# Kernel tuning notes

Measured on AMD Instinct MI355X. Metric: run time of the kernel, lower is better.

Reference implementation:

```python
import jax, jax.numpy as jnp
import numpy as np

# ---- static config (matches init_kwargs) ----
B = 32          # batch
CTX = 128       # context_dim
N_FRAMES = 128
N_SAMPLES = 32768
N_EVENTS = 16
CH = 256        # channels
WIN = 512       # window_size
HOP = WIN // 2  # 256
N_COEFFS = WIN // 2 + 1   # 257
TOTAL_COEFFS = N_COEFFS * 2  # 514


def _hann(n):
    # periodic Hann window (torch.hann_window default)
    i = jnp.arange(n, dtype=jnp.float32)
    return 0.5 * (1.0 - jnp.cos(2.0 * jnp.pi * i / n))


def _forward(param, times, noise, pos, proj_w, proj_b,
             w0, b0, w1, b1, w2, b2, w_out, b_out):
    # proj: [B, CTX] -> [B, CH]
    x = param @ proj_w.T + proj_b
    x = x[:, None, :] + pos                      # [B, N_FRAMES, CH] (pos broadcast)
    # LinearOutputStack: 3 hidden layers w/ leaky_relu(0.2), then output layer
    for w, b in ((w0, b0), (w1, b1), (w2, b2)):
        x = jax.nn.leaky_relu(x @ w.T + b, 0.2)
    x = x @ w_out.T + b_out                      # [B, N_FRAMES, 514]
    x = x.reshape(B, N_FRAMES, N_COEFFS, 2)
    mags = jnp.abs(x[..., 0])                    # [B, F, 257]
    phase = x[..., 1]
    # phase jitter: base phase of ones perturbed by uniform(-1,1) noise
    phase = 1.0 + phase * noise
    # mag/phase recomposition: per-frequency phase increment accumulated over frames
    freqs = jnp.linspace(0.0, 1.0, N_COEFFS)
    p = jnp.cumsum(phase * freqs * jnp.pi, axis=1)
    spec = mags * jnp.exp(1j * p)                # complex [B, F, 257]
    frames = jnp.fft.irfft(spec, n=WIN, axis=-1)  # [B, F, 512]
    frames = frames * _hann(WIN)
    total = (N_FRAMES - 1) * HOP + WIN
    idx = (jnp.arange(N_FRAMES) * HOP)[:, None] + jnp.arange(WIN)  # [F, 512]
    sig = jnp.zeros((B, total), frames.dtype).at[:, idx].add(frames)
    sig = sig[:, :N_SAMPLES]                     # [B, N_SAMPLES]
    # DiracScheduler (pre_sparse): upsample-with-holes frame-resolution diracs
    step = N_SAMPLES // N_FRAMES                 # 256
    up = jnp.zeros((B, N_EVENTS, N_SAMPLES), sig.dtype).at[:, :, ::step].set(times)
    # fft convolve event signal with dirac trains (zero-padded, linear conv)
    n2 = 2 * N_SAMPLES
    S = jnp.fft.rfft(sig, n=n2)[:, None, :]      # [B, 1, n2//2+1]
    T = jnp.fft.rfft(up, n=n2)                   # [B, E, n2//2+1]
    out = jnp.fft.irfft(S * T, n=n2)[..., :N_SAMPLES]
    return out                                   # [B, N_EVENTS, N_SAMPLES]


def setup_inputs() -> dict:
    key = jax.random.key(0)
    ks = jax.random.split(key, 16)
    s = 0.02
    param = jax.random.normal(ks[0], (B, CTX), jnp.float32)
    # sparse dirac times: one event position per (batch, event) at frame resolution
    posn = jax.random.randint(ks[1], (B, N_EVENTS), 0, N_FRAMES)
    amps = jax.random.uniform(ks[2], (B, N_EVENTS), jnp.float32, 0.1, 1.0)
    times = jax.nn.one_hot(posn, N_FRAMES, dtype=jnp.float32) * amps[..., None]
    noise = jax.random.uniform(ks[3], (B, N_FRAMES, N_COEFFS), jnp.float32, -1.0, 1.0)
    pos = jax.random.uniform(ks[4], (1, N_FRAMES, CH), jnp.float32, -0.01, 0.01)
    proj_w = jax.random.normal(ks[5], (CH, CTX), jnp.float32) * s
    proj_b = jnp.zeros((CH,), jnp.float32)
    w0 = jax.random.normal(ks[6], (CH, CH), jnp.float32) * s
    b0 = jnp.zeros((CH,), jnp.float32)
    w1 = jax.random.normal(ks[7], (CH, CH), jnp.float32) * s
    b1 = jnp.zeros((CH,), jnp.float32)
    w2 = jax.random.normal(ks[8], (CH, CH), jnp.float32) * s
    b2 = jnp.zeros((CH,), jnp.float32)
    w_out = jax.random.normal(ks[9], (TOTAL_COEFFS, CH), jnp.float32) * s
    b_out = jnp.zeros((TOTAL_COEFFS,), jnp.float32)
    return dict(param=param, times=times, noise=noise, pos=pos,
                proj_w=proj_w, proj_b=proj_b, w0=w0, b0=b0, w1=w1, b1=b1,
                w2=w2, b2=b2, w_out=w_out, b_out=b_out)


def reference(param, times, noise, pos, proj_w, proj_b,
              w0, b0, w1, b1, w2, b2, w_out, b_out):
    return _forward(param, times, noise, pos, proj_w, proj_b,
                    w0, b0, w1, b1, w2, b2, w_out, b_out)
```

## Files before the change

### kernel.cpp

```cpp
#include <hip/hip_runtime.h>
#include <cstddef>

typedef unsigned short u16;
typedef __bf16 bf16x8 __attribute__((ext_vector_type(8)));
typedef float f32x4 __attribute__((ext_vector_type(4)));

constexpr int B_   = 32;
constexpr int CTX_ = 128;
constexpr int NF_  = 128;
constexpr int NS_  = 32768;
constexpr int NE_  = 16;
constexpr int CH_  = 256;
constexpr int NC_  = 257;
constexpr int TC_  = 514;
constexpr int ROWS_ = B_ * NF_;
constexpr int CHUNK_ = 8;
constexpr int NCH_ = NF_ / CHUNK_;
constexpr int KE_ = 288;
constexpr int K3MLP_ = 768;
constexpr int K3IR_ = 896;
constexpr float PI_ = 3.14159265358979323846f;

__device__ __forceinline__ float lrelu(float v) { return v > 0.f ? v : 0.2f * v; }
__device__ __forceinline__ u16 f2bf(float x) {
    unsigned u = __float_as_uint(x);
    return (u16)((u + 0x7FFFu + ((u >> 16) & 1u)) >> 16);
}
__device__ __forceinline__ float bf2f(u16 h) { return __uint_as_float(((unsigned)h) << 16); }

__global__ __launch_bounds__(256) void prep_kernel(
    const float* __restrict__ param, const float* __restrict__ pw,
    const float* __restrict__ pb, const float* __restrict__ pos,
    const float* __restrict__ w0, const float* __restrict__ w1,
    const float* __restrict__ w2, const float* __restrict__ wo,
    const float* __restrict__ times,
    u16* __restrict__ Tt3, u16* __restrict__ W1_3, u16* __restrict__ W2_3,
    u16* __restrict__ WO_3, int* __restrict__ cnt, float2* __restrict__ taps,
    float* __restrict__ U, float* __restrict__ V)
{
    int blk = blockIdx.x;
    int tid = threadIdx.x;
    if (blk < 1792) {
        int idx = blk * 256 + tid;
        int z = idx / (256 * K3IR_);
        int r = idx - z * (256 * K3IR_);
        int n = r / K3IR_, col = r - n * K3IR_;
        u16 outv = 0;
        if (col < 864) {
            int seg = col / KE_;
            int j = col - seg * KE_;
            float val = 0.f;
            if (z == 0) {
                if (j < 129) {
                    int k = 2 * j;
                    float w = (k == 0 || k == 256) ? 1.f : 2.f;
                    int m = (k * n) & 511;
                    val = w * (1.f / 512.f) * cosf((float)m * (PI_ / 256.f));
                } else if (j < 258) {
                    int kk = 2 * (j - 129);
                    float w = (kk == 0 || kk == 256) ? 1.f : 2.f;
                    int m = (kk * n) & 511;
                    val = -w * (1.f / 512.f) * sinf((float)m * (PI_ / 256.f));
                }
            } else {
                if (j < 128) {
                    int k = 2 * j + 1;
                    int m = (k * n) & 511;
                    val = 2.f * (1.f / 512.f) * cosf((float)m * (PI_ / 256.f));
                } else if (j < 256) {
                    int kk = 2 * (j - 128) + 1;
                    int m = (kk * n) & 511;
                    val = -2.f * (1.f / 512.f) * sinf((float)m * (PI_ / 256.f));
                }
            }
            u16 h = f2bf(val);
            outv = (seg < 2) ? h : f2bf(val - bf2f(h));
        }
        Tt3[idx] = outv;
    } else if (blk < 2880) {
        int row = blk - 1792;
        int k = tid;
        float v;
        u16* p;
        if (row < 256) {
            v = w1[row * 256 + k];
            p = W1_3 + (size_t)row * K3MLP_;
        } else if (row < 512) {
            v = w2[(row - 256) * 256 + k];
            p = W2_3 + (size_t)(row - 256) * K3MLP_;
        } else {
            int n = row - 512;
            v = (n < TC_) ? wo[n * 256 + k] : 0.f;
            p = WO_3 + (size_t)n * K3MLP_;
        }
        u16 h = f2bf(v), lo = f2bf(v - bf2f(h));
        p[k] = h; p[256 + k] = h; p[512 + k] = lo;
    } else if (blk < 3392) {
        int be = blk - 2880;
        __shared__ int c;
        if (tid == 0) c = 0;
        __syncthreads();
        if (tid < NF_) {
            float v = times[(size_t)be * NF_ + tid];
            if (v != 0.f) {
                int slot = atomicAdd(&c, 1);
                taps[(size_t)be * NF_ + slot] = make_float2((float)tid, v);
            }
        }
        __syncthreads();
        if (tid == 0) cnt[be] = c;
    } else if (blk < 3424) {
        int b = blk - 3392;
        __shared__ float ly[256];
        {
            const float* pr = param + b * CTX_;
            const float* wr = pw + tid * CTX_;
            float s = 0.f;
            #pragma unroll 4
            for (int j = 0; j < CTX_; ++j) s += pr[j] * wr[j];
            ly[tid] = s + pb[tid];
        }
        __syncthreads();
        {
            const float* wn = w0 + tid * CH_;
            float s = 0.f;
            #pragma unroll 4
            for (int c2 = 0; c2 < CH_; ++c2) s += ly[c2] * wn[c2];
            U[b * CH_ + tid] = s;
        }
    } else {
        int f = blk - 3424;
        const float* pf = pos + f * CH_;
        const float* wn = w0 + tid * CH_;
        float s = 0.f;
        #pragma unroll 4
        for (int c2 = 0; c2 < CH_; ++c2) s += pf[c2] * wn[c2];
        V[f * CH_ + tid] = s;
    }
}

__global__ void fuse1_kernel(const float* __restrict__ U, const float* __restrict__ V,
                             const float* __restrict__ b0, u16* __restrict__ H3) {
    int idx = blockIdx.x * 256 + threadIdx.x;
    int c = idx & 255;
    int row = idx >> 8;
    int b = row >> 7, f = row & 127;
    float v = lrelu(U[b * CH_ + c] + V[f * CH_ + c] + b0[c]);
    u16 h = f2bf(v), lo = f2bf(v - bf2f(h));
    u16* p = H3 + (size_t)row * K3MLP_;
    p[c] = h; p[256 + c] = lo; p[512 + c] = h;
}

template<int EPI, int K3>
__global__ __launch_bounds__(128) void mfgemm(
    const u16* __restrict__ A3, const u16* __restrict__ B3,
    const float* __restrict__ bias, void* __restrict__ Cout,
    int N, int lda, int ldb, int ldc,
    size_t sAz, size_t sBz, size_t sCz)
{
    A3 += (size_t)blockIdx.z * sAz;
    B3 += (size_t)blockIdx.z * sBz;
    const int tid = threadIdx.x;
    const int m0 = blockIdx.y * 32, n0 = blockIdx.x * 64;
    __shared__ __align__(16) u16 Als[2 * 32 * 64];
    __shared__ __align__(16) u16 Bls[2 * 64 * 64];
    const int sr = tid >> 2;
    const int sc = (tid & 3) * 16;
    const u16* ga  = A3 + (size_t)(m0 + sr) * lda + sc;
    const u16* gb0 = B3 + (size_t)(n0 + sr) * ldb + sc;
    const u16* gb1 = B3 + (size_t)(n0 + 32 + sr) * ldb + sc;
    const int xr = (sr & 7) << 4;
    const int loA0 = sr * 128 + ((sc * 2) ^ xr);
    const int loA1 = sr * 128 + ((sc * 2 + 16) ^ xr);
    const int loB0 = sr * 128 + ((sc * 2) ^ xr);
    const int loB1 = sr * 128 + ((sc * 2 + 16) ^ xr);
    const int loB2 = (sr + 32) * 128 + ((sc * 2) ^ xr);
    const int loB3 = (sr + 32) * 128 + ((sc * 2 + 16) ^ xr);
    const int wv = tid >> 6, lane = tid & 63;
    const int wc = wv * 32;
    const int lr = lane & 15;
    const int lkb = (lane >> 4) * 16;
    const int xf = (lr & 7) << 4;
    const int raf0 = lr * 128, raf1 = (16 + lr) * 128;
    const int rbf0 = (wc + lr) * 128, rbf1 = (wc + 16 + lr) * 128;
    f32x4 acc00 = {0.f, 0.f, 0.f, 0.f}, acc01 = acc00, acc10 = acc00, acc11 = acc00;

    uint4 pa0, pa1, pb0, pb1, pb2, pb3;
    uint4 qa0, qa1, qb0, qb1, qb2, qb3;
    auto loadP = [&](int kt) {
        pa0 = *(const uint4*)(ga + kt);  pa1 = *(const uint4*)(ga + kt + 8);
        pb0 = *(const uint4*)(gb0 + kt); pb1 = *(const uint4*)(gb0 + kt + 8);
        pb2 = *(const uint4*)(gb1 + kt); pb3 = *(const uint4*)(gb1 + kt + 8);
    };
    auto loadQ = [&](int kt) {
        qa0 = *(const uint4*)(ga + kt);  qa1 = *(const uint4*)(ga + kt + 8);
        qb0 = *(const uint4*)(gb0 + kt); qb1 = *(const uint4*)(gb0 + kt + 8);
        qb2 = *(const uint4*)(gb1 + kt); qb3 = *(const uint4*)(gb1 + kt + 8);
    };
    auto compute = [&](int p) {
        const char* pa = (const char*)Als + p * 4096;
        const char* pb = (const char*)Bls + p * 8192;
        #pragma unroll
        for (int s = 0; s < 2; ++s) {
            int kb = (s * 64 + lkb) ^ xf;
            bf16x8 a0 = *(const bf16x8*)(pa + raf0 + kb);
            bf16x8 a1 = *(const bf16x8*)(pa + raf1 + kb);
            bf16x8 b0 = *(const bf16x8*)(pb + rbf0 + kb);
            bf16x8 b1 = *(const bf16x8*)(pb + rbf1 + kb);
            acc00 = __builtin_amdgcn_mfma_f32_16x16x32_bf16(a0, b0, acc00, 0, 0, 0);
            acc01 = __builtin_amdgcn_mfma_f32_16x16x32_bf16(a0, b1, acc01, 0, 0, 0);
            acc10 = __builtin_amdgcn_mfma_f32_16x16x32_bf16(a1, b0, acc10, 0, 0, 0);
            acc11 = __builtin_amdgcn_mfma_f32_16x16x32_bf16(a1, b1, acc11, 0, 0, 0);
        }
    };
    auto stage = [&](int p, const uint4& a0, const uint4& a1, const uint4& b0,
                     const uint4& b1, const uint4& b2, const uint4& b3) {
        char* ab = (char*)Als + p * 4096;
        char* bb = (char*)Bls + p * 8192;
        *(uint4*)(ab + loA0) = a0; *(uint4*)(ab + loA1) = a1;
        *(uint4*)(bb + loB0) = b0; *(uint4*)(bb + loB1) = b1;
        *(uint4*)(bb + loB2) = b2; *(uint4*)(bb + loB3) = b3;
    };
    loadP(0);
    loadQ(64);
    int p = 0;
    #pragma unroll
    for (int kt = 0; kt < K3; kt += 128) {
        stage(p, pa0, pa1, pb0, pb1, pb2, pb3);
        __syncthreads();
        if (kt + 128 < K3) loadP(kt + 128);
        compute(p);
        p ^= 1;
        stage(p, qa0, qa1, qb0, qb1, qb2, qb3);
        __syncthreads();
        if (kt + 192 < K3) loadQ(kt + 192);
        compute(p);
        p ^= 1;
    }
    const int er = (lane >> 4) * 4;
    const int ec = lane & 15;
    auto emit = [&](const f32x4& A, int mi, int ni) {
        #pragma unroll
        for (int r = 0; r < 4; ++r) {
            int m = m0 + mi * 16 + er + r;
            int n = n0 + wc + ni * 16 + ec;
            float v = A[r];
            if (EPI == 0) {
                v = lrelu(v + bias[n]);
                u16 h = f2bf(v), lo = f2bf(v - bf2f(h));
                u16* p2 = (u16*)Cout + (size_t)m * ldc + n;
                p2[0] = h; p2[256] = lo; p2[512] = h;
            } else if (EPI == 1) {
                if (n < N) ((float*)Cout)[(size_t)m * ldc + n] = v + bias[n];
            } else {
                float* cf = (float*)Cout + (size_t)blockIdx.z * sCz;
                cf[(size_t)m * ldc + n] = v;
            }
        }
    };
    emit(acc00, 0, 0); emit(acc01, 0, 1); emit(acc10, 1, 0); emit(acc11, 1, 1);
}

__global__ void scan1_kernel(const float* __restrict__ raw, const float* __restrict__ noise,
                             double* __restrict__ sums) {
    int b = blockIdx.x, c = blockIdx.y;
    int k = threadIdx.x;
    if (k >= NC_) return;
    float kf = (float)k * (PI_ / 256.f);
    double s = 0.0;
    #pragma unroll
    for (int j = 0; j < CHUNK_; ++j) {
        int row = b * NF_ + c * CHUNK_ + j;
        float2 v = *(const float2*)(raw + (size_t)row * TC_ + 2 * k);
        float d = (1.f + v.y * noise[(size_t)row * NC_ + k]) * kf;
        s += (double)d;
    }
    sums[((size_t)(b * NCH_ + c)) * NC_ + k] = s;
}

__global__ void scan2_kernel(const float* __restrict__ raw, const float* __restrict__ noise,
                             const double* __restrict__ sums,
                             u16* __restrict__ AB3e, u16* __restrict__ AB3o) {
    int b = blockIdx.x, c = blockIdx.y;
    int k = threadIdx.x;
    if (k >= NC_) {
        int t = k - NC_;
        for (int idx = t; idx < 250; idx += 63) {
            int col;
            u16* base;
            if (idx < 122) {
                col = (idx < 90) ? ((idx / 30) * KE_ + 258 + (idx % 30)) : (864 + (idx - 90));
                base = AB3e;
            } else {
                int u = idx - 122;
                col = (u < 96) ? ((u / 32) * KE_ + 256 + (u % 32)) : (864 + (u - 96));
                base = AB3o;
            }
            for (int j = 0; j < CHUNK_; ++j)
                base[(size_t)(b * NF_ + c * CHUNK_ + j) * K3IR_ + col] = 0;
        }
        return;
    }
    double p = 0.0;
    for (int cc = 0; cc < c; ++cc)
        p += sums[((size_t)(b * NCH_ + cc)) * NC_ + k];
    float kf = (float)k * (PI_ / 256.f);
    int half = k >> 1;
    bool even = (k & 1) == 0;
    int ccol = half;
    int scol = even ? (129 + half) : (128 + half);
    u16* dst = even ? AB3e : AB3o;
    for (int j = 0; j < CHUNK_; ++j) {
        int row = b * NF_ + c * CHUNK_ + j;
        float2 v = *(const float2*)(raw + (size_t)row * TC_ + 2 * k);
        float d = (1.f + v.y * noise[(size_t)row * NC_ + k]) * kf;
        p += (double)d;
        float m = fabsf(v.x);
        float sn, cs;
        sincosf((float)p, &sn, &cs);
        float a = m * cs, bb = m * sn;
        u16* pr = dst + (size_t)row * K3IR_;
        u16 ha = f2bf(a), la = f2bf(a - bf2f(ha));
        pr[ccol] = ha; pr[KE_ + ccol] = la; pr[2 * KE_ + ccol] = ha;
        u16 hb = f2bf(bb), lb = f2bf(bb - bf2f(hb));
        pr[scol] = hb; pr[KE_ + scol] = lb; pr[2 * KE_ + scol] = hb;
    }
}

__global__ __launch_bounds__(256) void conv2_kernel(const float* __restrict__ E,
                                                    const float* __restrict__ O,
                                                    const int* __restrict__ cnt,
                                                    const float2* __restrict__ taps,
                                                    float* __restrict__ out) {
    int be = blockIdx.y;
    int b = be >> 4;
    int n = cnt[be];
    int t = blockIdx.x * 2048 + (int)threadIdx.x * 8;
    int r0 = t & 255;
    float hr[8], hr2[8];
    #pragma unroll
    for (int j = 0; j < 8; ++j) {
        float cj = cosf((float)(r0 + j) * (PI_ / 256.f));
        hr[j]  = 0.5f - 0.5f * cj;
        hr2[j] = 0.5f + 0.5f * cj;
    }
    float acc[8] = {};
    for (int i = 0; i < n; ++i) {
        float2 ka = taps[(size_t)be * NF_ + i];
        int s0 = t - ((int)ka.x << 8);
        if (s0 < 0) continue;
        float amp = ka.y;
        int q = s0 >> 8;
        size_t row = (size_t)(b * NF_ + q) * 256 + r0;
        float4 e0 = *(const float4*)(E + row);
        float4 e1 = *(const float4*)(E + row + 4);
        float4 o0 = *(const float4*)(O + row);
        float4 o1 = *(const float4*)(O + row + 4);
        float sv[8];
        sv[0] = hr[0] * (e0.x + o0.x); sv[1] = hr[1] * (e0.y + o0.y);
        sv[2] = hr[2] * (e0.z + o0.z); sv[3] = hr[3] * (e0.w + o0.w);
        sv[4] = hr[4] * (e1.x + o1.x); sv[5] = hr[5] * (e1.y + o1.y);
        sv[6] = hr[6] * (e1.z + o1.z); sv[7] = hr[7] * (e1.w + o1.w);
        if (q > 0) {
            float4 pe0 = *(const float4*)(E + row - 256);
            float4 pe1 = *(const float4*)(E + row - 252);
            float4 po0 = *(const float4*)(O + row - 256);
            float4 po1 = *(const float4*)(O + row - 252);
            sv[0] += hr2[0] * (pe0.x - po0.x); sv[1] += hr2[1] * (pe0.y - po0.y);
            sv[2] += hr2[2] * (pe0.z - po0.z); sv[3] += hr2[3] * (pe0.w - po0.w);
            sv[4] += hr2[4] * (pe1.x - po1.x); sv[5] += hr2[5] * (pe1.y - po1.y);
            sv[6] += hr2[6] * (pe1.z - po1.z); sv[7] += hr2[7] * (pe1.w - po1.w);
        }
        #pragma unroll
        for (int j = 0; j < 8; ++j) acc[j] += amp * sv[j];
    }
    float* op = out + (size_t)be * NS_ + t;
    *(float4*)op = make_float4(acc[0], acc[1], acc[2], acc[3]);
    *(float4*)(op + 4) = make_float4(acc[4], acc[5], acc[6], acc[7]);
}

extern "C" void kernel_launch(void* const* d_in, const int* in_sizes, int n_in,
                              void* d_out, int out_size, void* d_ws, size_t ws_size,
                              hipStream_t stream) {
    const float* param  = (const float*)d_in[0];
    const float* times  = (const float*)d_in[1];
    const float* noise  = (const float*)d_in[2];
    const float* pos    = (const float*)d_in[3];
    const float* proj_w = (const float*)d_in[4];
    const float* proj_b = (const float*)d_in[5];
    const float* w0 = (const float*)d_in[6];
    const float* b0 = (const float*)d_in[7];
    const float* w1 = (const float*)d_in[8];
    const float* b1 = (const float*)d_in[9];
    const float* w2 = (const float*)d_in[10];
    const float* b2 = (const float*)d_in[11];
    const float* w_out = (const float*)d_in[12];
    const float* b_out = (const float*)d_in[13];
    float* out = (float*)d_out;
    float* ws = (float*)d_ws;

    constexpr size_t U_F    = 32 * 256;
    constexpr size_t V_F    = 128 * 256;
    constexpr size_t H3_F   = (size_t)ROWS_ * K3MLP_ / 2;
    constexpr size_t W3_F   = (size_t)256 * K3MLP_ / 2;
    constexpr size_t WO3_F  = (size_t)576 * K3MLP_ / 2;
    constexpr size_t RAW_F  = (size_t)ROWS_ * TC_;
    constexpr size_t AB3_F  = 2 * (size_t)ROWS_ * K3IR_ / 2;
    constexpr size_t TT3_F  = 2 * (size_t)256 * K3IR_ / 2;
    constexpr size_t EO_F   = 2 * (size_t)ROWS_ * 256;
    constexpr size_t SUMS_F = (size_t)B_ * NCH_ * NC_ * 2;

    size_t cur = 0;
    float* U    = ws + cur;                 cur += U_F;
    float* V    = ws + cur;                 cur += V_F;
    u16*  H1_3  = (u16*)(ws + cur);         cur += H3_F;
    u16*  H2_3  = (u16*)(ws + cur);         cur += H3_F;
    u16*  H3_3  = (u16*)(ws + cur);         cur += H3_F;
    u16*  W1_3  = (u16*)(ws + cur);         cur += W3_F;
    u16*  W2_3  = (u16*)(ws + cur);         cur += W3_F;
    u16*  WO_3  = (u16*)(ws + cur);         cur += WO3_F;
    float* RAW  = ws + cur;                 cur += RAW_F;
    u16*  AB3   = (u16*)(ws + cur);         cur += AB3_F;
    u16*  AB3e  = AB3;
    u16*  AB3o  = AB3 + (size_t)ROWS_ * K3IR_;
    u16*  Tt3   = (u16*)(ws + cur);         cur += TT3_F;
    float* EO   = ws + cur;                 cur += EO_F;
    double* SUMS = (double*)(ws + cur);     cur += SUMS_F;
    int*   CNT  = (int*)(ws + cur);         cur += 512;
    float2* TAPS = (float2*)(ws + cur);

    prep_kernel<<<3552, 256, 0, stream>>>(param, proj_w, proj_b, pos, w0, w1, w2, w_out,
                                          times, Tt3, W1_3, W2_3, WO_3, CNT, TAPS, U, V);
    fuse1_kernel<<<ROWS_ * CH_ / 256, 256, 0, stream>>>(U, V, b0, H1_3);
    mfgemm<0, K3MLP_><<<dim3(4, 128, 1), 128, 0, stream>>>(H1_3, W1_3, b1, H2_3, 256,
                                                           K3MLP_, K3MLP_, K3MLP_, 0, 0, 0);
    mfgemm<0, K3MLP_><<<dim3(4, 128, 1), 128, 0, stream>>>(H2_3, W2_3, b2, H3_3, 256,
                                                           K3MLP_, K3MLP_, K3MLP_, 0, 0, 0);
    mfgemm<1, K3MLP_><<<dim3(9, 128, 1), 128, 0, stream>>>(H3_3, WO_3, b_out, RAW, TC_,
                                                           K3MLP_, K3MLP_, TC_, 0, 0, 0);
    dim3 gS(B_, NCH_);
    scan1_kernel<<<gS, 320, 0, stream>>>(RAW, noise, SUMS);
    scan2_kernel<<<gS, 320, 0, stream>>>(RAW, noise, SUMS, AB3e, AB3o);
    mfgemm<2, K3IR_><<<dim3(4, 128, 2), 128, 0, stream>>>(AB3, Tt3, nullptr, EO, 256,
                                                          K3IR_, K3IR_, 256,
                                                          (size_t)ROWS_ * K3IR_,
                                                          (size_t)256 * K3IR_,
                                                          (size_t)ROWS_ * 256);
    dim3 gC(NS_ / 2048, B_ * NE_);
    conv2_kernel<<<gC, 256, 0, stream>>>(EO, EO + (size_t)ROWS_ * 256, CNT, TAPS, out);
}
```

Before: 106.4 us.

## Store split-bf16 operands as hi/lo pairs and synthesize the third K segment

The three-term split-bf16 GEMM operands (hi·hi + lo·hi + hi·lo) used to be stored physically tripled along K. They are now stored as just [hi, lo] per row, and the GEMM remaps the K index so the third segment re-reads the first A or B segment. This cuts workspace writes in the prep, scan and epilogue kernels and the global footprint the GEMMs read, while keeping the same MMA work. The IRFFT segment also grows from 288 to 320 columns, which adds padded K work. The twiddle table now uses a shared-memory cosine LUT instead of per-element sin/cos.

```diff
diff --git a/kernel.cpp b/kernel.cpp
--- a/kernel.cpp
+++ b/kernel.cpp
@@ -16,9 +16,12 @@
 constexpr int ROWS_ = B_ * NF_;
 constexpr int CHUNK_ = 8;
 constexpr int NCH_ = NF_ / CHUNK_;
-constexpr int KE_ = 288;
 constexpr int K3MLP_ = 768;
-constexpr int K3IR_ = 896;
+constexpr int SEGM_ = 256;
+constexpr int K3IR_ = 960;
+constexpr int SEGI_ = 320;
+constexpr int PIRW_ = 2 * SEGI_;
+constexpr int PMLW_ = 2 * SEGM_;
 constexpr float PI_ = 3.14159265358979323846f;
 
 __device__ __forceinline__ float lrelu(float v) { return v > 0.f ? v : 0.2f * v; }
@@ -34,69 +37,69 @@
     const float* __restrict__ w0, const float* __restrict__ w1,
     const float* __restrict__ w2, const float* __restrict__ wo,
     const float* __restrict__ times,
-    u16* __restrict__ Tt3, u16* __restrict__ W1_3, u16* __restrict__ W2_3,
-    u16* __restrict__ WO_3, int* __restrict__ cnt, float2* __restrict__ taps,
+    u16* __restrict__ Tt, u16* __restrict__ W1p, u16* __restrict__ W2p,
+    u16* __restrict__ WOp, int* __restrict__ cnt, float2* __restrict__ taps,
     float* __restrict__ U, float* __restrict__ V)
 {
     int blk = blockIdx.x;
     int tid = threadIdx.x;
-    if (blk < 1792) {
+    if (blk < 1280) {
+        __shared__ float lut[512];
+        lut[tid]       = cosf((float)tid * (PI_ / 256.f));
+        lut[tid + 256] = cosf((float)(tid + 256) * (PI_ / 256.f));
+        __syncthreads();
         int idx = blk * 256 + tid;
-        int z = idx / (256 * K3IR_);
-        int r = idx - z * (256 * K3IR_);
-        int n = r / K3IR_, col = r - n * K3IR_;
-        u16 outv = 0;
-        if (col < 864) {
-            int seg = col / KE_;
-            int j = col - seg * KE_;
-            float val = 0.f;
-            if (z == 0) {
-                if (j < 129) {
-                    int k = 2 * j;
-                    float w = (k == 0 || k == 256) ? 1.f : 2.f;
-                    int m = (k * n) & 511;
-                    val = w * (1.f / 512.f) * cosf((float)m * (PI_ / 256.f));
-                } else if (j < 258) {
-                    int kk = 2 * (j - 129);
-                    float w = (kk == 0 || kk == 256) ? 1.f : 2.f;
-                    int m = (kk * n) & 511;
-                    val = -w * (1.f / 512.f) * sinf((float)m * (PI_ / 256.f));
-                }
-            } else {
-                if (j < 128) {
-                    int k = 2 * j + 1;
-                    int m = (k * n) & 511;
-                    val = 2.f * (1.f / 512.f) * cosf((float)m * (PI_ / 256.f));
-                } else if (j < 256) {
-                    int kk = 2 * (j - 128) + 1;
-                    int m = (kk * n) & 511;
-                    val = -2.f * (1.f / 512.f) * sinf((float)m * (PI_ / 256.f));
-                }
+        int z = idx / (256 * PIRW_);
+        int r = idx - z * (256 * PIRW_);
+        int n = r / PIRW_, c = r - n * PIRW_;
+        bool hiplane = c < SEGI_;
+        int j = hiplane ? c : c - SEGI_;
+        float val = 0.f;
+        if (z == 0) {
+            if (j < 129) {
+                int k = 2 * j;
+                float w = (k == 0 || k == 256) ? 1.f : 2.f;
+                int m = (k * n) & 511;
+                val = w * (1.f / 512.f) * lut[m];
+            } else if (j < 258) {
+                int kk = 2 * (j - 129);
+                float w = (kk == 0 || kk == 256) ? 1.f : 2.f;
+                int m = (kk * n) & 511;
+                val = -w * (1.f / 512.f) * lut[(m - 128) & 511];
             }
-            u16 h = f2bf(val);
-            outv = (seg < 2) ? h : f2bf(val - bf2f(h));
-        }
-        Tt3[idx] = outv;
-    } else if (blk < 2880) {
-        int row = blk - 1792;
+        } else {
+            if (j < 128) {
+                int k = 2 * j + 1;
+                int m = (k * n) & 511;
+                val = 2.f * (1.f / 512.f) * lut[m];
+            } else if (j < 256) {
+                int kk = 2 * (j - 128) + 1;
+                int m = (kk * n) & 511;
+                val = -2.f * (1.f / 512.f) * lut[(m - 128) & 511];
+            }
+        }
+        u16 h = f2bf(val);
+        Tt[idx] = hiplane ? h : f2bf(val - bf2f(h));
+    } else if (blk < 2368) {
+        int row = blk - 1280;
         int k = tid;
         float v;
         u16* p;
         if (row < 256) {
             v = w1[row * 256 + k];
-            p = W1_3 + (size_t)row * K3MLP_;
+            p = W1p + (size_t)row * PMLW_;
         } else if (row < 512) {
             v = w2[(row - 256) * 256 + k];
-            p = W2_3 + (size_t)(row - 256) * K3MLP_;
+            p = W2p + (size_t)(row - 256) * PMLW_;
         } else {
             int n = row - 512;
             v = (n < TC_) ? wo[n * 256 + k] : 0.f;
-            p = WO_3 + (size_t)n * K3MLP_;
-        }
-        u16 h = f2bf(v), lo = f2bf(v - bf2f(h));
-        p[k] = h; p[256 + k] = h; p[512 + k] = lo;
-    } else if (blk < 3392) {
-        int be = blk - 2880;
+            p = WOp + (size_t)n * PMLW_;
+        }
+        u16 h = f2bf(v);
+        p[k] = h; p[256 + k] = f2bf(v - bf2f(h));
+    } else if (blk < 2880) {
+        int be = blk - 2368;
         __shared__ int c;
         if (tid == 0) c = 0;
         __syncthreads();
@@ -109,8 +112,8 @@
         }
         __syncthreads();
         if (tid == 0) cnt[be] = c;
-    } else if (blk < 3424) {
-        int b = blk - 3392;
+    } else if (blk < 2912) {
+        int b = blk - 2880;
         __shared__ float ly[256];
         {
             const float* pr = param + b * CTX_;
@@ -129,7 +132,7 @@
             U[b * CH_ + tid] = s;
         }
     } else {
-        int f = blk - 3424;
+        int f = blk - 2912;
         const float* pf = pos + f * CH_;
         const float* wn = w0 + tid * CH_;
         float s = 0.f;
@@ -140,24 +143,25 @@
 }
 
 __global__ void fuse1_kernel(const float* __restrict__ U, const float* __restrict__ V,
-                             const float* __restrict__ b0, u16* __restrict__ H3) {
+                             const float* __restrict__ b0, u16* __restrict__ Hp) {
     int idx = blockIdx.x * 256 + threadIdx.x;
     int c = idx & 255;
     int row = idx >> 8;
     int b = row >> 7, f = row & 127;
     float v = lrelu(U[b * CH_ + c] + V[f * CH_ + c] + b0[c]);
-    u16 h = f2bf(v), lo = f2bf(v - bf2f(h));
-    u16* p = H3 + (size_t)row * K3MLP_;
-    p[c] = h; p[256 + c] = lo; p[512 + c] = h;
-}
-
-template<int EPI, int K3>
+    u16 h = f2bf(v);
+    u16* p = Hp + (size_t)row * PMLW_;
+    p[c] = h; p[256 + c] = f2bf(v - bf2f(h));
+}
+
+template<int EPI, int K3, int SEG>
 __global__ __launch_bounds__(128) void mfgemm(
     const u16* __restrict__ A3, const u16* __restrict__ B3,
     const float* __restrict__ bias, void* __restrict__ Cout,
     int N, int lda, int ldb, int ldc,
     size_t sAz, size_t sBz, size_t sCz)
 {
+    constexpr int NSTEP = K3 / 64;
     A3 += (size_t)blockIdx.z * sAz;
     B3 += (size_t)blockIdx.z * sBz;
     const int tid = threadIdx.x;
@@ -172,8 +176,6 @@
     const int xr = (sr & 7) << 4;
     const int loA0 = sr * 128 + ((sc * 2) ^ xr);
     const int loA1 = sr * 128 + ((sc * 2 + 16) ^ xr);
-    const int loB0 = sr * 128 + ((sc * 2) ^ xr);
-    const int loB1 = sr * 128 + ((sc * 2 + 16) ^ xr);
     const int loB2 = (sr + 32) * 128 + ((sc * 2) ^ xr);
     const int loB3 = (sr + 32) * 128 + ((sc * 2 + 16) ^ xr);
     const int wv = tid >> 6, lane = tid & 63;
@@ -187,15 +189,19 @@
 
     uint4 pa0, pa1, pb0, pb1, pb2, pb3;
     uint4 qa0, qa1, qb0, qb1, qb2, qb3;
+    auto kA = [](int kt) { return kt >= 2 * SEG ? kt - 2 * SEG : kt; };
+    auto kB = [](int kt) { return kt >= SEG ? kt - SEG : kt; };
     auto loadP = [&](int kt) {
-        pa0 = *(const uint4*)(ga + kt);  pa1 = *(const uint4*)(ga + kt + 8);
-        pb0 = *(const uint4*)(gb0 + kt); pb1 = *(const uint4*)(gb0 + kt + 8);
-        pb2 = *(const uint4*)(gb1 + kt); pb3 = *(const uint4*)(gb1 + kt + 8);
+        int a = kA(kt), b = kB(kt);
+        pa0 = *(const uint4*)(ga + a);  pa1 = *(const uint4*)(ga + a + 8);
+        pb0 = *(const uint4*)(gb0 + b); pb1 = *(const uint4*)(gb0 + b + 8);
+        pb2 = *(const uint4*)(gb1 + b); pb3 = *(const uint4*)(gb1 + b + 8);
     };
     auto loadQ = [&](int kt) {
-        qa0 = *(const uint4*)(ga + kt);  qa1 = *(const uint4*)(ga + kt + 8);
-        qb0 = *(const uint4*)(gb0 + kt); qb1 = *(const uint4*)(gb0 + kt + 8);
-        qb2 = *(const uint4*)(gb1 + kt); qb3 = *(const uint4*)(gb1 + kt + 8);
+        int a = kA(kt), b = kB(kt);
+        qa0 = *(const uint4*)(ga + a);  qa1 = *(const uint4*)(ga + a + 8);
+        qb0 = *(const uint4*)(gb0 + b); qb1 = *(const uint4*)(gb0 + b + 8);
+        qb2 = *(const uint4*)(gb1 + b); qb3 = *(const uint4*)(gb1 + b + 8);
     };
     auto compute = [&](int p) {
         const char* pa = (const char*)Als + p * 4096;
@@ -218,23 +224,25 @@
         char* ab = (char*)Als + p * 4096;
         char* bb = (char*)Bls + p * 8192;
         *(uint4*)(ab + loA0) = a0; *(uint4*)(ab + loA1) = a1;
-        *(uint4*)(bb + loB0) = b0; *(uint4*)(bb + loB1) = b1;
+        *(uint4*)(bb + loA0) = b0; *(uint4*)(bb + loA1) = b1;
         *(uint4*)(bb + loB2) = b2; *(uint4*)(bb + loB3) = b3;
     };
     loadP(0);
-    loadQ(64);
+    if (NSTEP > 1) loadQ(64);
     int p = 0;
     #pragma unroll
-    for (int kt = 0; kt < K3; kt += 128) {
-        stage(p, pa0, pa1, pb0, pb1, pb2, pb3);
-        __syncthreads();
-        if (kt + 128 < K3) loadP(kt + 128);
-        compute(p);
-        p ^= 1;
-        stage(p, qa0, qa1, qb0, qb1, qb2, qb3);
-        __syncthreads();
-        if (kt + 192 < K3) loadQ(kt + 192);
-        compute(p);
+    for (int i = 0; i < NSTEP; ++i) {
+        if ((i & 1) == 0) {
+            stage(p, pa0, pa1, pb0, pb1, pb2, pb3);
+            __syncthreads();
+            if (i + 2 < NSTEP) loadP((i + 2) * 64);
+            compute(p);
+        } else {
+            stage(p, qa0, qa1, qb0, qb1, qb2, qb3);
+            __syncthreads();
+            if (i + 2 < NSTEP) loadQ((i + 2) * 64);
+            compute(p);
+        }
         p ^= 1;
     }
     const int er = (lane >> 4) * 4;
@@ -247,9 +255,9 @@
             float v = A[r];
             if (EPI == 0) {
                 v = lrelu(v + bias[n]);
-                u16 h = f2bf(v), lo = f2bf(v - bf2f(h));
+                u16 h = f2bf(v);
                 u16* p2 = (u16*)Cout + (size_t)m * ldc + n;
-                p2[0] = h; p2[256] = lo; p2[512] = h;
+                p2[0] = h; p2[256] = f2bf(v - bf2f(h));
             } else if (EPI == 1) {
                 if (n < N) ((float*)Cout)[(size_t)m * ldc + n] = v + bias[n];
             } else {
@@ -280,24 +288,20 @@
 
 __global__ void scan2_kernel(const float* __restrict__ raw, const float* __restrict__ noise,
                              const double* __restrict__ sums,
-                             u16* __restrict__ AB3e, u16* __restrict__ AB3o) {
+                             u16* __restrict__ ABe, u16* __restrict__ ABo) {
     int b = blockIdx.x, c = blockIdx.y;
     int k = threadIdx.x;
     if (k >= NC_) {
         int t = k - NC_;
-        for (int idx = t; idx < 250; idx += 63) {
+        for (int idx = t; idx < 252; idx += 63) {
             int col;
             u16* base;
-            if (idx < 122) {
-                col = (idx < 90) ? ((idx / 30) * KE_ + 258 + (idx % 30)) : (864 + (idx - 90));
-                base = AB3e;
-            } else {
-                int u = idx - 122;
-                col = (u < 96) ? ((u / 32) * KE_ + 256 + (u % 32)) : (864 + (u - 96));
-                base = AB3o;
-            }
+            if (idx < 62)       { col = 258 + idx;              base = ABe; }
+            else if (idx < 124) { col = SEGI_ + 258 + (idx - 62);  base = ABe; }
+            else if (idx < 188) { col = 256 + (idx - 124);       base = ABo; }
+            else                { col = SEGI_ + 256 + (idx - 188); base = ABo; }
             for (int j = 0; j < CHUNK_; ++j)
-                base[(size_t)(b * NF_ + c * CHUNK_ + j) * K3IR_ + col] = 0;
+                base[(size_t)(b * NF_ + c * CHUNK_ + j) * PIRW_ + col] = 0;
         }
         return;
     }
@@ -309,7 +313,7 @@
     bool even = (k & 1) == 0;
     int ccol = half;
     int scol = even ? (129 + half) : (128 + half);
-    u16* dst = even ? AB3e : AB3o;
+    u16* dst = even ? ABe : ABo;
     for (int j = 0; j < CHUNK_; ++j) {
         int row = b * NF_ + c * CHUNK_ + j;
         float2 v = *(const float2*)(raw + (size_t)row * TC_ + 2 * k);
@@ -319,11 +323,11 @@
         float sn, cs;
         sincosf((float)p, &sn, &cs);
         float a = m * cs, bb = m * sn;
-        u16* pr = dst + (size_t)row * K3IR_;
-        u16 ha = f2bf(a), la = f2bf(a - bf2f(ha));
-        pr[ccol] = ha; pr[KE_ + ccol] = la; pr[2 * KE_ + ccol] = ha;
-        u16 hb = f2bf(bb), lb = f2bf(bb - bf2f(hb));
-        pr[scol] = hb; pr[KE_ + scol] = lb; pr[2 * KE_ + scol] = hb;
+        u16* pr = dst + (size_t)row * PIRW_;
+        u16 ha = f2bf(a);
+        pr[ccol] = ha; pr[SEGI_ + ccol] = f2bf(a - bf2f(ha));
+        u16 hb = f2bf(bb);
+        pr[scol] = hb; pr[SEGI_ + scol] = f2bf(bb - bf2f(hb));
     }
 }
 
@@ -401,51 +405,51 @@
 
     constexpr size_t U_F    = 32 * 256;
     constexpr size_t V_F    = 128 * 256;
-    constexpr size_t H3_F   = (size_t)ROWS_ * K3MLP_ / 2;
-    constexpr size_t W3_F   = (size_t)256 * K3MLP_ / 2;
-    constexpr size_t WO3_F  = (size_t)576 * K3MLP_ / 2;
+    constexpr size_t HP_F   = (size_t)ROWS_ * PMLW_ / 2;
+    constexpr size_t W_F    = (size_t)256 * PMLW_ / 2;
+    constexpr size_t WO_F   = (size_t)576 * PMLW_ / 2;
     constexpr size_t RAW_F  = (size_t)ROWS_ * TC_;
-    constexpr size_t AB3_F  = 2 * (size_t)ROWS_ * K3IR_ / 2;
-    constexpr size_t TT3_F  = 2 * (size_t)256 * K3IR_ / 2;
+    constexpr size_t ABP_F  = 2 * (size_t)ROWS_ * PIRW_ / 2;
+    constexpr size_t TTP_F  = 2 * (size_t)256 * PIRW_ / 2;
     constexpr size_t EO_F   = 2 * (size_t)ROWS_ * 256;
     constexpr size_t SUMS_F = (size_t)B_ * NCH_ * NC_ * 2;
 
     size_t cur = 0;
     float* U    = ws + cur;                 cur += U_F;
     float* V    = ws + cur;                 cur += V_F;
-    u16*  H1_3  = (u16*)(ws + cur);         cur += H3_F;
-    u16*  H2_3  = (u16*)(ws + cur);         cur += H3_F;
-    u16*  H3_3  = (u16*)(ws + cur);         cur += H3_F;
-    u16*  W1_3  = (u16*)(ws + cur);         cur += W3_F;
-    u16*  W2_3  = (u16*)(ws + cur);         cur += W3_F;
-    u16*  WO_3  = (u16*)(ws + cur);         cur += WO3_F;
+    u16*  H1p   = (u16*)(ws + cur);         cur += HP_F;
+    u16*  H2p   = (u16*)(ws + cur);         cur += HP_F;
+    u16*  H3p   = (u16*)(ws + cur);         cur += HP_F;
+    u16*  W1p   = (u16*)(ws + cur);         cur += W_F;
+    u16*  W2p   = (u16*)(ws + cur);         cur += W_F;
+    u16*  WOp   = (u16*)(ws + cur);         cur += WO_F;
     float* RAW  = ws + cur;                 cur += RAW_F;
-    u16*  AB3   = (u16*)(ws + cur);         cur += AB3_F;
-    u16*  AB3e  = AB3;
-    u16*  AB3o  = AB3 + (size_t)ROWS_ * K3IR_;
-    u16*  Tt3   = (u16*)(ws + cur);         cur += TT3_F;
+    u16*  ABP   = (u16*)(ws + cur);         cur += ABP_F;
+    u16*  ABe   = ABP;
+    u16*  ABo   = ABP + (size_t)ROWS_ * PIRW_;
+    u16*  TTP   = (u16*)(ws + cur);         cur += TTP_F;
     float* EO   = ws + cur;                 cur += EO_F;
     double* SUMS = (double*)(ws + cur);     cur += SUMS_F;
     int*   CNT  = (int*)(ws + cur);         cur += 512;
     float2* TAPS = (float2*)(ws + cur);
 
-    prep_kernel<<<3552, 256, 0, stream>>>(param, proj_w, proj_b, pos, w0, w1, w2, w_out,
-                                          times, Tt3, W1_3, W2_3, WO_3, CNT, TAPS, U, V);
-    fuse1_kernel<<<ROWS_ * CH_ / 256, 256, 0, stream>>>(U, V, b0, H1_3);
-    mfgemm<0, K3MLP_><<<dim3(4, 128, 1), 128, 0, stream>>>(H1_3, W1_3, b1, H2_3, 256,
-                                                           K3MLP_, K3MLP_, K3MLP_, 0, 0, 0);
-    mfgemm<0, K3MLP_><<<dim3(4, 128, 1), 128, 0, stream>>>(H2_3, W2_3, b2, H3_3, 256,
-                                                           K3MLP_, K3MLP_, K3MLP_, 0, 0, 0);
-    mfgemm<1, K3MLP_><<<dim3(9, 128, 1), 128, 0, stream>>>(H3_3, WO_3, b_out, RAW, TC_,
-                                                           K3MLP_, K3MLP_, TC_, 0, 0, 0);
+    prep_kernel<<<3040, 256, 0, stream>>>(param, proj_w, proj_b, pos, w0, w1, w2, w_out,
+                                          times, TTP, W1p, W2p, WOp, CNT, TAPS, U, V);
+    fuse1_kernel<<<ROWS_ * CH_ / 256, 256, 0, stream>>>(U, V, b0, H1p);
+    mfgemm<0, K3MLP_, SEGM_><<<dim3(4, 128, 1), 128, 0, stream>>>(H1p, W1p, b1, H2p, 256,
+                                                                  PMLW_, PMLW_, PMLW_, 0, 0, 0);
+    mfgemm<0, K3MLP_, SEGM_><<<dim3(4, 128, 1), 128, 0, stream>>>(H2p, W2p, b2, H3p, 256,
+                                                                  PMLW_, PMLW_, PMLW_, 0, 0, 0);
+    mfgemm<1, K3MLP_, SEGM_><<<dim3(9, 128, 1), 128, 0, stream>>>(H3p, WOp, b_out, RAW, TC_,
+                                                                  PMLW_, PMLW_, TC_, 0, 0, 0);
     dim3 gS(B_, NCH_);
     scan1_kernel<<<gS, 320, 0, stream>>>(RAW, noise, SUMS);
-    scan2_kernel<<<gS, 320, 0, stream>>>(RAW, noise, SUMS, AB3e, AB3o);
-    mfgemm<2, K3IR_><<<dim3(4, 128, 2), 128, 0, stream>>>(AB3, Tt3, nullptr, EO, 256,
-                                                          K3IR_, K3IR_, 256,
-                                                          (size_t)ROWS_ * K3IR_,
-                                                          (size_t)256 * K3IR_,
-                                                          (size_t)ROWS_ * 256);
+    scan2_kernel<<<gS, 320, 0, stream>>>(RAW, noise, SUMS, ABe, ABo);
+    mfgemm<2, K3IR_, SEGI_><<<dim3(4, 128, 2), 128, 0, stream>>>(ABP, TTP, nullptr, EO, 256,
+                                                                 PIRW_, PIRW_, 256,
+                                                                 (size_t)ROWS_ * PIRW_,
+                                                                 (size_t)256 * PIRW_,
+                                                                 (size_t)ROWS_ * 256);
     dim3 gC(NS_ / 2048, B_ * NE_);
     conv2_kernel<<<gC, 256, 0, stream>>>(EO, EO + (size_t)ROWS_ * 256, CNT, TAPS, out);
 }
```

New measurement: 95.11 us. 10.6% less time.
